# Kernel tuning notes

Measured on AMD Instinct MI355X. Metric: run time of the kernel, lower is better.

## Reference

```python
import jax, jax.numpy as jnp
import numpy as np

HIDDEN = 2048
NUM_OPS = 3
BATCH = 16384


def setup_inputs() -> dict:
    key = jax.random.key(0)
    ks = jax.random.split(key, 6)
    x = jax.random.normal(ks[0], (BATCH, HIDDEN), dtype=jnp.float32)
    chosen_ops = jax.random.randint(ks[1], (BATCH,), 0, NUM_OPS, dtype=jnp.int32)
    # Stacked expert params; torch nn.Linear computes x @ W.T + b, W: [out, in].
    # We store W already transposed to [in, out] for direct einsum.
    scale = 1.0 / np.sqrt(HIDDEN)
    W1 = jax.random.uniform(ks[2], (NUM_OPS, HIDDEN, HIDDEN), jnp.float32, -scale, scale)
    b1 = jax.random.uniform(ks[3], (NUM_OPS, HIDDEN), jnp.float32, -scale, scale)
    W2 = jax.random.uniform(ks[4], (NUM_OPS, HIDDEN, HIDDEN), jnp.float32, -scale, scale)
    b2 = jax.random.uniform(ks[5], (NUM_OPS, HIDDEN), jnp.float32, -scale, scale)
    return {"x": x, "W1": W1, "b1": b1, "W2": W2, "b2": b2, "chosen_ops": chosen_ops}


def reference(x, W1, b1, W2, b2, chosen_ops):
    # Temper.apply_operators: each row of x is routed to one expert MLP:
    #   out[i] = relu(W2_e @ relu(W1_e @ x[i] + b1_e) + b2_e), e = chosen_ops[i]
    # operator_freshness starts at zeros, so the +0.01*result branch is inactive.
    # Vectorized: run all experts on all rows (small fixed NUM_OPS), then select.
    h = jax.nn.relu(jnp.einsum('bh,ehk->ebk', x, W1) + b1[:, None, :])   # [E,B,H]
    y = jax.nn.relu(jnp.einsum('ebh,ehk->ebk', h, W2) + b2[:, None, :])  # [E,B,H]
    out = y[chosen_ops, jnp.arange(x.shape[0]), :]                        # [B,H]
    return out
```

## Files before the change

### kernel.cpp

```cpp
#include <hip/hip_runtime.h>
#include <hip/hip_bf16.h>
#include <stdint.h>

#define HIDDEN 2048
#define BATCH 16384
#define NUM_OPS 3
#define NT_M 67
#define M_CAP (NT_M * 256)
#define NXT 8
#define KT 32

typedef __attribute__((ext_vector_type(4))) float f32x4;
typedef __attribute__((ext_vector_type(8))) short short8;
typedef __attribute__((ext_vector_type(8))) __bf16 bf16x8;

static constexpr size_t XB_SZ   = (size_t)M_CAP * HIDDEN * 2;
static constexpr size_t H_SZ    = XB_SZ;
static constexpr size_t WT_SZ   = (size_t)NUM_OPS * HIDDEN * HIDDEN * 2;
static constexpr size_t PERM_SZ = (size_t)M_CAP * 4;

__device__ __forceinline__ unsigned f2bf(float f) {
  unsigned u = __float_as_uint(f);
  return (u + 0x7FFFu + ((u >> 16) & 1u)) >> 16;
}

__device__ __forceinline__ void async_ld16(const void* g, void* l) {
  __builtin_amdgcn_global_load_lds(
      (__attribute__((address_space(1))) void*)(void*)g,
      (__attribute__((address_space(3))) void*)l, 16, 0, 0);
}

__global__ __launch_bounds__(256) void k_count(const int* __restrict__ ops,
                                               int* __restrict__ cnt,
                                               int* __restrict__ perm) {
  int i = blockIdx.x * 256 + threadIdx.x;
  if (i < M_CAP) perm[i] = -1;
  int e = (i < BATCH) ? ops[i] : -1;
  int lane = threadIdx.x & 63;
#pragma unroll
  for (int ee = 0; ee < NUM_OPS; ee++) {
    unsigned long long m = __ballot(e == ee);
    if (lane == 0 && m) atomicAdd(&cnt[ee], __popcll(m));
  }
}

__global__ void k_scan(const int* __restrict__ cnt, int* __restrict__ seg,
                       int* __restrict__ te) {
  int a0 = (cnt[0] + 255) & ~255;
  int a1 = (cnt[1] + 255) & ~255;
  int a2 = (cnt[2] + 255) & ~255;
  if (threadIdx.x == 0) {
    seg[0] = 0; seg[1] = a0; seg[2] = a0 + a1; seg[3] = a0 + a1 + a2;
  }
  for (int t = threadIdx.x; t < NT_M; t += 64) {
    int row = t * 256;
    int ex = -1;
    if (row < a0) ex = 0;
    else if (row < a0 + a1) ex = 1;
    else if (row < a0 + a1 + a2) ex = 2;
    te[t] = ex;
  }
}

__global__ __launch_bounds__(256) void k_perm(const int* __restrict__ ops,
                                              const int* __restrict__ seg,
                                              int* __restrict__ c2,
                                              int* __restrict__ perm) {
  int b = blockIdx.x * 256 + threadIdx.x;
  int e = (b < BATCH) ? ops[b] : -1;
  int lane = threadIdx.x & 63;
#pragma unroll
  for (int ee = 0; ee < NUM_OPS; ee++) {
    unsigned long long m = __ballot(e == ee);
    if (m) {
      int base = 0;
      if (lane == 0) base = atomicAdd(&c2[ee], __popcll(m));
      base = __shfl(base, 0);
      if (e == ee) {
        int myoff = __popcll(m & ((1ull << lane) - 1ull));
        perm[seg[ee] + base + myoff] = b;
      }
    }
  }
}

__global__ __launch_bounds__(256) void k_prep(const float* __restrict__ x,
                                              const int* __restrict__ perm,
                                              short* __restrict__ xb,
                                              const float* __restrict__ W1,
                                              const float* __restrict__ W2,
                                              short* __restrict__ W1t,
                                              short* __restrict__ W2t) {
  int tid = threadIdx.x;
  if (blockIdx.x < M_CAP) {
    int pos = blockIdx.x;
    int b = perm[pos];
    uint4 o;
    if (b < 0) {
      o = make_uint4(0u, 0u, 0u, 0u);
    } else {
      const float4* xs = (const float4*)(x + (size_t)b * HIDDEN + tid * 8);
      float4 f0 = xs[0], f1 = xs[1];
      o.x = f2bf(f0.x) | (f2bf(f0.y) << 16);
      o.y = f2bf(f0.z) | (f2bf(f0.w) << 16);
      o.z = f2bf(f1.x) | (f2bf(f1.y) << 16);
      o.w = f2bf(f1.z) | (f2bf(f1.w) << 16);
    }
    *(uint4*)(xb + (size_t)pos * HIDDEN + tid * 8) = o;
  } else {
    __shared__ float t[64][65];
    int q = blockIdx.x - M_CAP;
    int z = q >> 10;
    int rem = q & 1023;
    int by = rem >> 5, bx = rem & 31;
    const float* src = (z < 3) ? (W1 + (size_t)z * HIDDEN * HIDDEN)
                               : (W2 + (size_t)(z - 3) * HIDDEN * HIDDEN);
    short* dst = (z < 3) ? (W1t + (size_t)z * HIDDEN * HIDDEN)
                         : (W2t + (size_t)(z - 3) * HIDDEN * HIDDEN);
    int k0 = by * 64;
    int n0 = bx * 64;
    {
      int kk = tid >> 4, n4 = (tid & 15) * 4;
#pragma unroll
      for (int p = 0; p < 4; p++) {
        int k = p * 16 + kk;
        *(float4*)&t[k][n4] = *(const float4*)&src[(size_t)(k0 + k) * HIDDEN + n0 + n4];
      }
    }
    __syncthreads();
#pragma unroll
    for (int p = 0; p < 2; p++) {
      int qq = p * 256 + tid;
      int n = qq >> 3, uc = qq & 7;
      uint4 o;
      unsigned* po = (unsigned*)&o;
#pragma unroll
      for (int j = 0; j < 4; j++) {
        float a = t[uc * 8 + 2 * j][n];
        float c = t[uc * 8 + 2 * j + 1][n];
        po[j] = f2bf(a) | (f2bf(c) << 16);
      }
      *(uint4*)&dst[(size_t)(n0 + n) * HIDDEN + k0 + uc * 8] = o;
    }
  }
}

template <int SECOND>
__global__ __launch_bounds__(512, 2)
void gemm256(const short* __restrict__ A, const short* __restrict__ Wt,
             const float* __restrict__ bias, const int* __restrict__ te,
             const int* __restrict__ perm, short* __restrict__ Hout,
             float* __restrict__ Yout) {
  extern __shared__ short lds[];

  const int lin = blockIdx.x;
  const int xt = lin & 7;
  const int yt = lin >> 3;
  const int e = te[yt];
  if (e < 0) return;

  const int tid = threadIdx.x;
  const int wid = tid >> 6;
  const int lane = tid & 63;
  const int quad = lane >> 4;
  const int l16 = lane & 15;
  const int wmh = wid >> 2;
  const int wnq = wid & 3;
  const int brow0 = (wnq & 1) * 64;

  const short* Ag = A + (size_t)yt * 256 * HIDDEN;
  const short* Bg = Wt + (size_t)e * HIDDEN * HIDDEN + (size_t)xt * 256 * HIDDEN;

  const int r0 = tid >> 3;
  const int c0 = ((tid & 7) ^ (r0 & 7)) * 8;
  const short* pA = Ag + (size_t)r0 * HIDDEN + c0;
  const short* pB = Bg + (size_t)r0 * HIDDEN + c0;
  const int dstw = wid * 512;

  auto stage = [&](const short* src, int dst) {
    async_ld16(src, lds + dst + dstw);
    async_ld16(src + 64 * HIDDEN, lds + dst + 4096 + dstw);
  };
  auto frag = [&](int base, int r, int q) {
    return __builtin_bit_cast(bf16x8,
        *(const short8*)(lds + base + r * 64 + ((q ^ (r & 7)) * 8)));
  };

  f32x4 acc[8][4] = {};
  bf16x8 af[4][2], bA[2][2], bB[2][2];

  stage(pA, 0);
  stage(pA + 128 * HIDDEN, 8192);
  stage(pB, 16384);
  stage(pB + 128 * HIDDEN, 24576);
  stage(pB + 64, 32768 + 16384);
  stage(pB + 64 + 128 * HIDDEN, 32768 + 24576);
  asm volatile("s_waitcnt vmcnt(4)" ::: "memory");
  __builtin_amdgcn_s_barrier();

  for (int t = 0; t < KT; ++t) {
    const int b = (t & 1) << 15;
    const int nb = 32768 - b;
    const int aMy = b + wmh * 8192;
    const int bMy = b + 16384 + (wnq >> 1) * 8192;
    const short* pAn = pA + (t + 1) * 64;
    const short* pBn = pB + (t + 2) * 64;

#pragma unroll
    for (int i = 0; i < 4; ++i)
#pragma unroll
      for (int s = 0; s < 2; ++s)
        af[i][s] = frag(aMy, i * 16 + l16, s * 4 + quad);
#pragma unroll
    for (int j = 0; j < 2; ++j)
#pragma unroll
      for (int s = 0; s < 2; ++s)
        bA[j][s] = frag(bMy, brow0 + j * 16 + l16, s * 4 + quad);
    if (t + 1 < KT) stage(pAn, nb);
    __builtin_amdgcn_sched_barrier(0);
    __builtin_amdgcn_s_barrier();
    asm volatile("s_waitcnt lgkmcnt(0)" ::: "memory");
    __builtin_amdgcn_sched_barrier(0);
    __builtin_amdgcn_s_setprio(1);
#pragma unroll
    for (int i = 0; i < 4; ++i)
#pragma unroll
      for (int j = 0; j < 2; ++j)
#pragma unroll
        for (int s = 0; s < 2; ++s)
          acc[i][j] = __builtin_amdgcn_mfma_f32_16x16x32_bf16(af[i][s], bA[j][s], acc[i][j], 0, 0, 0);
    __builtin_amdgcn_s_setprio(0);
    __builtin_amdgcn_sched_barrier(0);
    __builtin_amdgcn_s_barrier();

#pragma unroll
    for (int j = 0; j < 2; ++j)
#pragma unroll
      for (int s = 0; s < 2; ++s)
        bB[j][s] = frag(bMy, brow0 + 32 + j * 16 + l16, s * 4 + quad);
    if (t + 1 < KT) stage(pAn + 128 * HIDDEN, nb + 8192);
    __builtin_amdgcn_sched_barrier(0);
    __builtin_amdgcn_s_barrier();
    asm volatile("s_waitcnt lgkmcnt(0)" ::: "memory");
    __builtin_amdgcn_sched_barrier(0);
    __builtin_amdgcn_s_setprio(1);
#pragma unroll
    for (int i = 0; i < 4; ++i)
#pragma unroll
      for (int j = 0; j < 2; ++j)
#pragma unroll
        for (int s = 0; s < 2; ++s)
          acc[i][2 + j] = __builtin_amdgcn_mfma_f32_16x16x32_bf16(af[i][s], bB[j][s], acc[i][2 + j], 0, 0, 0);
    __builtin_amdgcn_s_setprio(0);
    __builtin_amdgcn_sched_barrier(0);
    __builtin_amdgcn_s_barrier();

#pragma unroll
    for (int i = 0; i < 4; ++i)
#pragma unroll
      for (int s = 0; s < 2; ++s)
        af[i][s] = frag(aMy, 64 + i * 16 + l16, s * 4 + quad);
    if (t + 2 < KT) stage(pBn, b + 16384);
    __builtin_amdgcn_sched_barrier(0);
    __builtin_amdgcn_s_barrier();
    asm volatile("s_waitcnt lgkmcnt(0)" ::: "memory");
    __builtin_amdgcn_sched_barrier(0);
    __builtin_amdgcn_s_setprio(1);
#pragma unroll
    for (int i = 0; i < 4; ++i)
#pragma unroll
      for (int j = 0; j < 2; ++j)
#pragma unroll
        for (int s = 0; s < 2; ++s)
          acc[4 + i][2 + j] = __builtin_amdgcn_mfma_f32_16x16x32_bf16(af[i][s], bB[j][s], acc[4 + i][2 + j], 0, 0, 0);
    __builtin_amdgcn_s_setprio(0);
    __builtin_amdgcn_sched_barrier(0);
    __builtin_amdgcn_s_barrier();

    if (t + 2 < KT) stage(pBn + 128 * HIDDEN, b + 24576);
    __builtin_amdgcn_sched_barrier(0);
    __builtin_amdgcn_s_barrier();
    __builtin_amdgcn_s_setprio(1);
#pragma unroll
    for (int i = 0; i < 4; ++i)
#pragma unroll
      for (int j = 0; j < 2; ++j)
#pragma unroll
        for (int s = 0; s < 2; ++s)
          acc[4 + i][j] = __builtin_amdgcn_mfma_f32_16x16x32_bf16(af[i][s], bA[j][s], acc[4 + i][j], 0, 0, 0);
    __builtin_amdgcn_s_setprio(0);
    __builtin_amdgcn_sched_barrier(0);
    if (t + 2 < KT) asm volatile("s_waitcnt vmcnt(4)" ::: "memory");
    else            asm volatile("s_waitcnt vmcnt(0)" ::: "memory");
    __builtin_amdgcn_s_barrier();
  }

  const int rb = yt * 256 + wmh * 128 + quad * 4;
  const int cb = xt * 256 + wnq * 64 + l16;
#pragma unroll
  for (int i = 0; i < 8; ++i) {
#pragma unroll
    for (int r = 0; r < 4; ++r) {
      const int m = rb + i * 16 + r;
      int bidx = 0;
      if (SECOND) bidx = perm[m];
#pragma unroll
      for (int j = 0; j < 4; ++j) {
        const int n = cb + j * 16;
        float v = acc[i][j][r] + bias[e * HIDDEN + n];
        v = v > 0.0f ? v : 0.0f;
        if (SECOND) {
          if (bidx >= 0) Yout[(size_t)bidx * HIDDEN + n] = v;
        } else {
          Hout[(size_t)m * HIDDEN + n] = (short)f2bf(v);
        }
      }
    }
  }
}

extern "C" void kernel_launch(void* const* d_in, const int* in_sizes, int n_in,
                              void* d_out, int out_size, void* d_ws, size_t ws_size,
                              hipStream_t stream) {
  const float* x  = (const float*)d_in[0];
  const float* W1 = (const float*)d_in[1];
  const float* b1 = (const float*)d_in[2];
  const float* W2 = (const float*)d_in[3];
  const float* b2 = (const float*)d_in[4];
  const int* ops  = (const int*)d_in[5];
  float* out = (float*)d_out;

  char* ws = (char*)d_ws;
  short* xb  = (short*)(ws);
  short* h   = (short*)(ws + XB_SZ);
  short* w1t = (short*)(ws + XB_SZ + H_SZ);
  short* w2t = (short*)(ws + XB_SZ + H_SZ + WT_SZ);
  int* perm  = (int*)(ws + XB_SZ + H_SZ + 2 * WT_SZ);
  int* meta  = (int*)(ws + XB_SZ + H_SZ + 2 * WT_SZ + PERM_SZ);
  int* cnt = meta;
  int* c2  = meta + 4;
  int* seg = meta + 8;
  int* te  = meta + 16;

  static bool attr_done = false;
  if (!attr_done) {
    hipFuncSetAttribute((const void*)gemm256<0>,
                        hipFuncAttributeMaxDynamicSharedMemorySize, 131072);
    hipFuncSetAttribute((const void*)gemm256<1>,
                        hipFuncAttributeMaxDynamicSharedMemorySize, 131072);
    attr_done = true;
  }

  hipMemsetAsync(meta, 0, 32, stream);
  k_count<<<(M_CAP + 255) / 256, 256, 0, stream>>>(ops, cnt, perm);
  k_scan<<<1, 64, 0, stream>>>(cnt, seg, te);
  k_perm<<<BATCH / 256, 256, 0, stream>>>(ops, seg, c2, perm);
  k_prep<<<M_CAP + 6 * 32 * 32, 256, 0, stream>>>(x, perm, xb, W1, W2, w1t, w2t);
  gemm256<0><<<NXT * NT_M, 512, 131072, stream>>>(xb, w1t, b1, te, perm, h, nullptr);
  gemm256<1><<<NXT * NT_M, 512, 131072, stream>>>(h, w2t, b2, te, perm, nullptr, out);
}
```

Measured before the change: 675.3 us.

## Shrink GEMM tile to 256x128 with triple-buffered LDS pipeline

Changes the grouped GEMM tile from 256x256 to 256x128 (16 N-tiles instead of 8) and gives each wave a 64x64 sub-tile. The two-stage double buffer becomes a three-stage LDS ring (24 KB per stage, 144 KB total) that prefetches two K-steps ahead, with two MFMA phases per step instead of four. The goal is to hide global load latency better and add more blocks for load balance. The cost is lower arithmetic intensity per block and more total A-tile traffic, and the larger LDS footprint likely allows only one block per CU despite launch_bounds(512,2).

Result: no change. 677.1 us (+0.3%).

```diff
diff --git a/kernel.cpp b/kernel.cpp
--- a/kernel.cpp
+++ b/kernel.cpp
@@ -7,7 +7,7 @@
 #define NUM_OPS 3
 #define NT_M 67
 #define M_CAP (NT_M * 256)
-#define NXT 8
+#define NXT 16
 #define KT 32
 
 typedef __attribute__((ext_vector_type(4))) float f32x4;
@@ -154,8 +154,8 @@
   extern __shared__ short lds[];
 
   const int lin = blockIdx.x;
-  const int xt = lin & 7;
-  const int yt = lin >> 3;
+  const int xt = lin & 15;
+  const int yt = lin >> 4;
   const int e = te[yt];
   if (e < 0) return;
 
@@ -164,12 +164,11 @@
   const int lane = tid & 63;
   const int quad = lane >> 4;
   const int l16 = lane & 15;
-  const int wmh = wid >> 2;
-  const int wnq = wid & 3;
-  const int brow0 = (wnq & 1) * 64;
+  const int wm64 = (wid >> 1) * 64;
+  const int bn64 = (wid & 1) * 64;
 
   const short* Ag = A + (size_t)yt * 256 * HIDDEN;
-  const short* Bg = Wt + (size_t)e * HIDDEN * HIDDEN + (size_t)xt * 256 * HIDDEN;
+  const short* Bg = Wt + (size_t)e * HIDDEN * HIDDEN + (size_t)xt * 128 * HIDDEN;
 
   const int r0 = tid >> 3;
   const int c0 = ((tid & 7) ^ (r0 & 7)) * 8;
@@ -177,46 +176,44 @@
   const short* pB = Bg + (size_t)r0 * HIDDEN + c0;
   const int dstw = wid * 512;
 
-  auto stage = [&](const short* src, int dst) {
-    async_ld16(src, lds + dst + dstw);
-    async_ld16(src + 64 * HIDDEN, lds + dst + 4096 + dstw);
+  auto stageA01 = [&](int sb, int k0) {
+    async_ld16(pA + k0,                lds + sb + dstw);
+    async_ld16(pA + 64 * HIDDEN + k0,  lds + sb + 4096 + dstw);
+  };
+  auto stageA23 = [&](int sb, int k0) {
+    async_ld16(pA + 128 * HIDDEN + k0, lds + sb + 8192 + dstw);
+    async_ld16(pA + 192 * HIDDEN + k0, lds + sb + 12288 + dstw);
+  };
+  auto stageB0 = [&](int sb, int k0) {
+    async_ld16(pB + k0,                lds + sb + 16384 + dstw);
+  };
+  auto stageB1 = [&](int sb, int k0) {
+    async_ld16(pB + 64 * HIDDEN + k0,  lds + sb + 20480 + dstw);
   };
   auto frag = [&](int base, int r, int q) {
     return __builtin_bit_cast(bf16x8,
         *(const short8*)(lds + base + r * 64 + ((q ^ (r & 7)) * 8)));
   };
 
-  f32x4 acc[8][4] = {};
-  bf16x8 af[4][2], bA[2][2], bB[2][2];
-
-  stage(pA, 0);
-  stage(pA + 128 * HIDDEN, 8192);
-  stage(pB, 16384);
-  stage(pB + 128 * HIDDEN, 24576);
-  stage(pB + 64, 32768 + 16384);
-  stage(pB + 64 + 128 * HIDDEN, 32768 + 24576);
-  asm volatile("s_waitcnt vmcnt(4)" ::: "memory");
+  f32x4 acc[4][4] = {};
+  bf16x8 af[4], bfr[4];
+
+  int cur = 0, nxt = 24576, stg = 49152;
+
+  stageA01(cur, 0); stageA23(cur, 0); stageB0(cur, 0); stageB1(cur, 0);
+  stageA01(nxt, 64); stageA23(nxt, 64); stageB0(nxt, 64); stageB1(nxt, 64);
+  asm volatile("s_waitcnt vmcnt(6)" ::: "memory");
   __builtin_amdgcn_s_barrier();
 
   for (int t = 0; t < KT; ++t) {
-    const int b = (t & 1) << 15;
-    const int nb = 32768 - b;
-    const int aMy = b + wmh * 8192;
-    const int bMy = b + 16384 + (wnq >> 1) * 8192;
-    const short* pAn = pA + (t + 1) * 64;
-    const short* pBn = pB + (t + 2) * 64;
-
-#pragma unroll
-    for (int i = 0; i < 4; ++i)
-#pragma unroll
-      for (int s = 0; s < 2; ++s)
-        af[i][s] = frag(aMy, i * 16 + l16, s * 4 + quad);
-#pragma unroll
-    for (int j = 0; j < 2; ++j)
-#pragma unroll
-      for (int s = 0; s < 2; ++s)
-        bA[j][s] = frag(bMy, brow0 + j * 16 + l16, s * 4 + quad);
-    if (t + 1 < KT) stage(pAn, nb);
+    const int k2 = (t + 2) * 64;
+    const bool pf = (t + 2 < KT);
+
+#pragma unroll
+    for (int i = 0; i < 4; ++i) af[i]  = frag(cur,        wm64 + i * 16 + l16, quad);
+#pragma unroll
+    for (int j = 0; j < 4; ++j) bfr[j] = frag(cur + 16384, bn64 + j * 16 + l16, quad);
+    if (pf) { stageA01(stg, k2); stageB0(stg, k2); }
     __builtin_amdgcn_sched_barrier(0);
     __builtin_amdgcn_s_barrier();
     asm volatile("s_waitcnt lgkmcnt(0)" ::: "memory");
@@ -225,20 +222,17 @@
 #pragma unroll
     for (int i = 0; i < 4; ++i)
 #pragma unroll
-      for (int j = 0; j < 2; ++j)
-#pragma unroll
-        for (int s = 0; s < 2; ++s)
-          acc[i][j] = __builtin_amdgcn_mfma_f32_16x16x32_bf16(af[i][s], bA[j][s], acc[i][j], 0, 0, 0);
+      for (int j = 0; j < 4; ++j)
+        acc[i][j] = __builtin_amdgcn_mfma_f32_16x16x32_bf16(af[i], bfr[j], acc[i][j], 0, 0, 0);
     __builtin_amdgcn_s_setprio(0);
     __builtin_amdgcn_sched_barrier(0);
     __builtin_amdgcn_s_barrier();
 
 #pragma unroll
-    for (int j = 0; j < 2; ++j)
-#pragma unroll
-      for (int s = 0; s < 2; ++s)
-        bB[j][s] = frag(bMy, brow0 + 32 + j * 16 + l16, s * 4 + quad);
-    if (t + 1 < KT) stage(pAn + 128 * HIDDEN, nb + 8192);
+    for (int i = 0; i < 4; ++i) af[i]  = frag(cur,        wm64 + i * 16 + l16, 4 + quad);
+#pragma unroll
+    for (int j = 0; j < 4; ++j) bfr[j] = frag(cur + 16384, bn64 + j * 16 + l16, 4 + quad);
+    if (pf) { stageA23(stg, k2); stageB1(stg, k2); }
     __builtin_amdgcn_sched_barrier(0);
     __builtin_amdgcn_s_barrier();
     asm volatile("s_waitcnt lgkmcnt(0)" ::: "memory");
@@ -247,58 +241,21 @@
 #pragma unroll
     for (int i = 0; i < 4; ++i)
 #pragma unroll
-      for (int j = 0; j < 2; ++j)
-#pragma unroll
-        for (int s = 0; s < 2; ++s)
-          acc[i][2 + j] = __builtin_amdgcn_mfma_f32_16x16x32_bf16(af[i][s], bB[j][s], acc[i][2 + j], 0, 0, 0);
+      for (int j = 0; j < 4; ++j)
+        acc[i][j] = __builtin_amdgcn_mfma_f32_16x16x32_bf16(af[i], bfr[j], acc[i][j], 0, 0, 0);
     __builtin_amdgcn_s_setprio(0);
     __builtin_amdgcn_sched_barrier(0);
+    if (pf) asm volatile("s_waitcnt vmcnt(6)" ::: "memory");
+    else    asm volatile("s_waitcnt vmcnt(0)" ::: "memory");
     __builtin_amdgcn_s_barrier();
 
-#pragma unroll
-    for (int i = 0; i < 4; ++i)
-#pragma unroll
-      for (int s = 0; s < 2; ++s)
-        af[i][s] = frag(aMy, 64 + i * 16 + l16, s * 4 + quad);
-    if (t + 2 < KT) stage(pBn, b + 16384);
-    __builtin_amdgcn_sched_barrier(0);
-    __builtin_amdgcn_s_barrier();
-    asm volatile("s_waitcnt lgkmcnt(0)" ::: "memory");
-    __builtin_amdgcn_sched_barrier(0);
-    __builtin_amdgcn_s_setprio(1);
-#pragma unroll
-    for (int i = 0; i < 4; ++i)
-#pragma unroll
-      for (int j = 0; j < 2; ++j)
-#pragma unroll
-        for (int s = 0; s < 2; ++s)
-          acc[4 + i][2 + j] = __builtin_amdgcn_mfma_f32_16x16x32_bf16(af[i][s], bB[j][s], acc[4 + i][2 + j], 0, 0, 0);
-    __builtin_amdgcn_s_setprio(0);
-    __builtin_amdgcn_sched_barrier(0);
-    __builtin_amdgcn_s_barrier();
-
-    if (t + 2 < KT) stage(pBn + 128 * HIDDEN, b + 24576);
-    __builtin_amdgcn_sched_barrier(0);
-    __builtin_amdgcn_s_barrier();
-    __builtin_amdgcn_s_setprio(1);
-#pragma unroll
-    for (int i = 0; i < 4; ++i)
-#pragma unroll
-      for (int j = 0; j < 2; ++j)
-#pragma unroll
-        for (int s = 0; s < 2; ++s)
-          acc[4 + i][j] = __builtin_amdgcn_mfma_f32_16x16x32_bf16(af[i][s], bA[j][s], acc[4 + i][j], 0, 0, 0);
-    __builtin_amdgcn_s_setprio(0);
-    __builtin_amdgcn_sched_barrier(0);
-    if (t + 2 < KT) asm volatile("s_waitcnt vmcnt(4)" ::: "memory");
-    else            asm volatile("s_waitcnt vmcnt(0)" ::: "memory");
-    __builtin_amdgcn_s_barrier();
-  }
-
-  const int rb = yt * 256 + wmh * 128 + quad * 4;
-  const int cb = xt * 256 + wnq * 64 + l16;
-#pragma unroll
-  for (int i = 0; i < 8; ++i) {
+    int tmp = cur; cur = nxt; nxt = stg; stg = tmp;
+  }
+
+  const int rb = yt * 256 + wm64 + quad * 4;
+  const int cb = xt * 128 + bn64 + l16;
+#pragma unroll
+  for (int i = 0; i < 4; ++i) {
 #pragma unroll
     for (int r = 0; r < 4; ++r) {
       const int m = rb + i * 16 + r;
@@ -345,9 +302,9 @@
   static bool attr_done = false;
   if (!attr_done) {
     hipFuncSetAttribute((const void*)gemm256<0>,
-                        hipFuncAttributeMaxDynamicSharedMemorySize, 131072);
+                        hipFuncAttributeMaxDynamicSharedMemorySize, 147456);
     hipFuncSetAttribute((const void*)gemm256<1>,
-                        hipFuncAttributeMaxDynamicSharedMemorySize, 131072);
+                        hipFuncAttributeMaxDynamicSharedMemorySize, 147456);
     attr_done = true;
   }
 
@@ -356,6 +313,6 @@
   k_scan<<<1, 64, 0, stream>>>(cnt, seg, te);
   k_perm<<<BATCH / 256, 256, 0, stream>>>(ops, seg, c2, perm);
   k_prep<<<M_CAP + 6 * 32 * 32, 256, 0, stream>>>(x, perm, xb, W1, W2, w1t, w2t);
-  gemm256<0><<<NXT * NT_M, 512, 131072, stream>>>(xb, w1t, b1, te, perm, h, nullptr);
-  gemm256<1><<<NXT * NT_M, 512, 131072, stream>>>(h, w2t, b2, te, perm, nullptr, out);
-}
+  gemm256<0><<<NXT * NT_M, 512, 147456, stream>>>(xb, w1t, b1, te, perm, h, nullptr);
+  gemm256<1><<<NXT * NT_M, 512, 147456, stream>>>(h, w2t, b2, te, perm, nullptr, out);
+}
```
